# Performance work log

Measured on AMD Instinct MI355X. Metric: run time of the kernel, lower is better.

Reference implementation:

```python
import jax, jax.numpy as jnp
import numpy as np

B, T, E = 4, 2_000_000, 8
C, K, STRIDE = 128, 512, 512
CHUNK, OVERLAP = 64000, 511  # overlap defaults to kernel_size - 1


def _candidate_positions(T):
    """Exact set of window start positions visited by the chunked streaming max.

    Replays the chunk loop of _lowmem_max_over_time: chunk starts advance by
    step = chunk_size - overlap (not a multiple of stride!), and within each
    chunk conv windows start at chunk_start + stride*k.
    """
    step = max(1, CHUNK - OVERLAP)
    pos = []
    start = 0
    while start < T:
        end = min(start + CHUNK, T)
        end_ext = min(end + OVERLAP, T)
        L = end_ext - start
        if L >= K:
            n = (L - K) // STRIDE + 1
            pos.append(start + STRIDE * np.arange(n, dtype=np.int64))
        if end == T:
            break
        start += step
    p = np.unique(np.concatenate(pos))
    return np.clip(p, 0, max(0, T - K))


POS = _candidate_positions(T)                       # [P] static window starts
WIN_IDX = POS[:, None] + np.arange(K, dtype=np.int64)  # [P, K] gather indices


def setup_inputs() -> dict:
    key = jax.random.key(0)
    ks = jax.random.split(key, 5)
    scale = 1.0 / float(np.sqrt(E * K))  # torch Conv1d default init range
    return {
        "x": jax.random.normal(ks[0], (B, T, E), dtype=jnp.float32),
        "w1": jax.random.uniform(ks[1], (C, E, K), jnp.float32, -scale, scale),
        "b1": jax.random.uniform(ks[2], (C,), jnp.float32, -scale, scale),
        "w2": jax.random.uniform(ks[3], (C, E, K), jnp.float32, -scale, scale),
        "b2": jax.random.uniform(ks[4], (C,), jnp.float32, -scale, scale),
    }


def reference(x, w1, b1, w2, b2):
    # Gather every candidate window the chunked scan would see: [B, P, K, E]
    wins = x[:, WIN_IDX, :]
    # Original clones windows under no_grad (stop_grad_input=True): input gets no grad.
    wins = jax.lax.stop_gradient(wins)
    # Gated conv (GLU): conv1(z) * sigmoid(conv2(z)) at each window -> [B, C, P]
    c1 = jnp.einsum('bpke,cek->bcp', wins, w1) + b1[:, None]
    c2 = jnp.einsum('bpke,cek->bcp', wins, w2) + b2[:, None]
    g = c1 * jax.nn.sigmoid(c2)
    # Global max-over-time per (batch, channel); identical value to the
    # running-max pass followed by exact re-evaluation at argmax positions.
    return g.max(axis=-1)  # [B, C]
```

## Files before the change

### kernel.cpp

```cpp
#include <hip/hip_runtime.h>


#define T_LEN 2000000
#define P_CNT 3937
#define M_TOT 15748
#define KD    4096

typedef __attribute__((ext_vector_type(8))) short short8;
typedef __attribute__((ext_vector_type(4))) float f32x4;

static __device__ __forceinline__ unsigned short f2bf(float f) {
    unsigned u = __builtin_bit_cast(unsigned, f);
    unsigned r = (u + 0x7FFFu + ((u >> 16) & 1u)) >> 16;
    return (unsigned short)r;
}

static __device__ __forceinline__ unsigned ordenc(float f) {
    unsigned u = __builtin_bit_cast(unsigned, f);
    return (u & 0x80000000u) ? ~u : (u | 0x80000000u);
}

static __device__ __forceinline__ size_t row_base_bp(int bb, int p) {
    int j, kp;
    if (p < 3875) { j = p / 125; kp = p - j * 125; }
    else          { j = 31;      kp = p - 3875; }
    long pos = (long)j * 63489 + (long)kp * 512;
    return ((size_t)bb * T_LEN + (size_t)pos) * 8u;
}

static __device__ __forceinline__ uint2 cvt4(float4 v) {
    unsigned lo, hi;
    asm("v_cvt_pk_bf16_f32 %0, %1, %2" : "=v"(lo) : "v"(v.x), "v"(v.y));
    asm("v_cvt_pk_bf16_f32 %0, %1, %2" : "=v"(hi) : "v"(v.z), "v"(v.w));
    uint2 u; u.x = lo; u.y = hi;
    return u;
}

__global__ __launch_bounds__(256) void pack_w(const float* __restrict__ w1,
                                              const float* __restrict__ w2,
                                              uint4* __restrict__ Bpf,
                                              unsigned* __restrict__ outu) {
    int c = blockIdx.x * 256 + threadIdx.x;
    if (c < 512) outu[c] = 0u;
    if (c >= 131072) return;
    int l  = c & 63;
    int w  = (c >> 6) & 15;
    int kq = (c >> 10) & 1;
    int ks = c >> 11;
    int cl = l & 15;
    int n  = (cl < 8) ? (w * 8 + cl) : (128 + w * 8 + (cl - 8));
    int kb = ks * 64 + kq * 32 + ((l >> 4) << 3);
    const float* src = (n < 128) ? w1 : w2;
    int cc = n & 127;
    unsigned short h[8];
#pragma unroll
    for (int j = 0; j < 8; ++j) {
        int k = kb + j;
        h[j] = f2bf(src[cc * 4096 + (k & 7) * 512 + (k >> 3)]);
    }
    uint4 v;
    v.x = (unsigned)h[0] | ((unsigned)h[1] << 16);
    v.y = (unsigned)h[2] | ((unsigned)h[3] << 16);
    v.z = (unsigned)h[4] | ((unsigned)h[5] << 16);
    v.w = (unsigned)h[6] | ((unsigned)h[7] << 16);
    Bpf[c] = v;
}

#define LOAD_B(BB, KS)                                                         \
    do {                                                                       \
        _Pragma("unroll")                                                      \
        for (int kq = 0; kq < 2; ++kq)                                         \
            BB[kq] = Bq[((KS) * 2 + kq) * 1024 + bbase];                       \
    } while (0)

#define STEP(KS, BCUR, BNXT)                                                   \
    do {                                                                       \
        const int ks_ = (KS);                                                  \
        const int ksn = (ks_ + 1 < 64) ? ks_ + 1 : 63;                         \
        LOAD_B(BNXT, ksn);                                                     \
        const int ksl = (ks_ + 4 < 64) ? ks_ + 4 : 63;                         \
        float4 aF = *(const float4*)(x + aoff + (size_t)(ksl * 64));           \
        const char* As = smem + (ks_ & 3) * 8192;                              \
        _Pragma("unroll")                                                      \
        for (int kq = 0; kq < 2; ++kq) {                                       \
            short8 b = __builtin_bit_cast(short8, BCUR[kq]);                   \
            _Pragma("unroll")                                                  \
            for (int mf = 0; mf < 4; ++mf) {                                   \
                short8 af = *(const short8*)(As + aro[kq][mf]);                \
                acc[mf] = __builtin_amdgcn_mfma_f32_16x16x32_bf16(             \
                    af, b, acc[mf], 0, 0, 0);                                  \
            }                                                                  \
        }                                                                      \
        *(uint2*)(smem + ((ks_ + 2) & 3) * 8192 + awb) = cvt4(aA);             \
        aA = aB; aB = aF;                                                      \
        asm volatile("s_waitcnt lgkmcnt(0)" ::: "memory");                     \
        __builtin_amdgcn_s_barrier();                                          \
        asm volatile("" ::: "memory");                                         \
    } while (0)

__global__ __launch_bounds__(1024, 4) void gemm_max(const float* __restrict__ x,
                                                    const uint4* __restrict__ Bq,
                                                    const float* __restrict__ b1,
                                                    const float* __restrict__ b2,
                                                    unsigned* __restrict__ outu) {
    __shared__ __align__(16) char smem[32768];

    const int t    = threadIdx.x;
    const int lane = t & 63;
    const int w    = t >> 6;
    const int bid  = blockIdx.x;
    const int bb   = bid / 62;
    const int p0   = (bid % 62) * 64;

    const int rowS = t >> 4;
    const int kcS  = t & 15;
    int pS = p0 + rowS; if (pS > P_CNT - 1) pS = P_CNT - 1;
    const size_t aoff = row_base_bp(bb, pS) + (size_t)(kcS * 4);
    const int    awb  = (rowS * 128 + kcS * 8) ^ ((rowS & 7) << 4);

    int aro[2][2 * 2];
#pragma unroll
    for (int kq = 0; kq < 2; ++kq)
#pragma unroll
        for (int mf = 0; mf < 4; ++mf) {
            int row = mf * 16 + (lane & 15);
            aro[kq][mf] = (row * 128 + kq * 64 + (lane >> 4) * 16)
                          ^ ((row & 7) << 4);
        }

    const int bbase = w * 64 + lane;

#pragma unroll
    for (int pt = 0; pt < 2; ++pt) {
        float4 v = *(const float4*)(x + aoff + pt * 64);
        *(uint2*)(smem + pt * 8192 + awb) = cvt4(v);
    }
    __syncthreads();

    float4 aA = *(const float4*)(x + aoff + 128);
    float4 aB = *(const float4*)(x + aoff + 192);
    uint4 BX[2], BY[2];
    LOAD_B(BX, 0);

    f32x4 acc[4];
#pragma unroll
    for (int mf = 0; mf < 4; ++mf) acc[mf] = (f32x4){0.f, 0.f, 0.f, 0.f};

    for (int ks = 0; ks < 64; ks += 2) {
        STEP(ks, BX, BY);
        STEP(ks + 1, BY, BX);
    }

    const int   cidx = w * 8 + (lane & 7);
    const float bb1  = b1[cidx];
    const float bb2  = b2[cidx];
    float best = -3.4e38f;
#pragma unroll
    for (int mf = 0; mf < 4; ++mf)
#pragma unroll
        for (int q = 0; q < 4; ++q) {
            float v  = acc[mf][q];
            float ov = __shfl_xor(v, 8);
            float c1 = v + bb1;
            float c2 = ov + bb2;
            float g  = c1 / (1.f + __expf(-c2));
            best = fmaxf(best, g);
        }
    best = fmaxf(best, __shfl_xor(best, 16));
    best = fmaxf(best, __shfl_xor(best, 32));
    if (lane < 8)
        atomicMax(&outu[bb * 128 + w * 8 + lane], ordenc(best));
}

__global__ __launch_bounds__(256) void unmap_out(unsigned* __restrict__ outu) {
    int i = blockIdx.x * 256 + threadIdx.x;
    if (i < 512) {
        unsigned u = outu[i];
        outu[i] = (u & 0x80000000u) ? (u ^ 0x80000000u) : ~u;
    }
}

extern "C" void kernel_launch(void* const* d_in, const int* in_sizes, int n_in,
                              void* d_out, int out_size, void* d_ws, size_t ws_size,
                              hipStream_t stream) {
    const float* x  = (const float*)d_in[0];
    const float* w1 = (const float*)d_in[1];
    const float* b1 = (const float*)d_in[2];
    const float* w2 = (const float*)d_in[3];
    const float* b2 = (const float*)d_in[4];

    uint4*    Bpf  = (uint4*)d_ws;
    unsigned* outu = (unsigned*)d_out;

    pack_w<<<dim3(512), dim3(256), 0, stream>>>(w1, w2, Bpf, outu);

    const int nblk = 62 * 4;
    gemm_max<<<dim3(nblk), dim3(1024), 0, stream>>>(x, (const uint4*)Bpf, b1, b2, outu);

    unmap_out<<<dim3(2), dim3(256), 0, stream>>>(outu);
}
```

Baseline: 70.91 us.

## Switch GEMM to 32x32x16 bf16 MFMA with 2x8 wave tiling

Replaces the per-wave four 16x16x32 MFMAs over 64 rows by 8 columns with a single 32x32x16 MFMA accumulator tile covering 32 rows by 32 columns (16 conv1 plus 16 conv2 channels). The weight packing layout, B fragment loads, A LDS offsets and the GLU/max epilogue are rewritten to match. The larger MFMA shape is meant to reduce LDS A-fragment reads per FLOP and instruction issue overhead. In exchange each wave now loads twice as many B fragments per k-step, since B is shared across the two row groups instead of A being shared across waves.

Result: slower. 93.44 us (+31.8%).

```diff
diff --git a/kernel.cpp b/kernel.cpp
--- a/kernel.cpp
+++ b/kernel.cpp
@@ -7,7 +7,7 @@
 #define KD    4096
 
 typedef __attribute__((ext_vector_type(8))) short short8;
-typedef __attribute__((ext_vector_type(4))) float f32x4;
+typedef __attribute__((ext_vector_type(16))) float f32x16;
 
 static __device__ __forceinline__ unsigned short f2bf(float f) {
     unsigned u = __builtin_bit_cast(unsigned, f);
@@ -43,13 +43,14 @@
     int c = blockIdx.x * 256 + threadIdx.x;
     if (c < 512) outu[c] = 0u;
     if (c >= 131072) return;
-    int l  = c & 63;
-    int w  = (c >> 6) & 15;
-    int kq = (c >> 10) & 1;
-    int ks = c >> 11;
-    int cl = l & 15;
-    int n  = (cl < 8) ? (w * 8 + cl) : (128 + w * 8 + (cl - 8));
-    int kb = ks * 64 + kq * 32 + ((l >> 4) << 3);
+    int l    = c & 63;
+    int g    = (c >> 6) & 7;
+    int s    = (c >> 9) & 3;
+    int ks   = c >> 11;
+    int cl   = l & 31;
+    int half = l >> 5;
+    int n  = (cl < 16) ? (g * 16 + cl) : (128 + g * 16 + (cl - 16));
+    int kb = ks * 64 + s * 16 + half * 8;
     const float* src = (n < 128) ? w1 : w2;
     int cc = n & 127;
     unsigned short h[8];
@@ -69,8 +70,8 @@
 #define LOAD_B(BB, KS)                                                         \
     do {                                                                       \
         _Pragma("unroll")                                                      \
-        for (int kq = 0; kq < 2; ++kq)                                         \
-            BB[kq] = Bq[((KS) * 2 + kq) * 1024 + bbase];                       \
+        for (int s = 0; s < 4; ++s)                                            \
+            BB[s] = Bq[((KS) * 4 + s) * 512 + bbase];                          \
     } while (0)
 
 #define STEP(KS, BCUR, BNXT)                                                   \
@@ -82,14 +83,10 @@
         float4 aF = *(const float4*)(x + aoff + (size_t)(ksl * 64));           \
         const char* As = smem + (ks_ & 3) * 8192;                              \
         _Pragma("unroll")                                                      \
-        for (int kq = 0; kq < 2; ++kq) {                                       \
-            short8 b = __builtin_bit_cast(short8, BCUR[kq]);                   \
-            _Pragma("unroll")                                                  \
-            for (int mf = 0; mf < 4; ++mf) {                                   \
-                short8 af = *(const short8*)(As + aro[kq][mf]);                \
-                acc[mf] = __builtin_amdgcn_mfma_f32_16x16x32_bf16(             \
-                    af, b, acc[mf], 0, 0, 0);                                  \
-            }                                                                  \
+        for (int s = 0; s < 4; ++s) {                                          \
+            short8 af = *(const short8*)(As + aro[s]);                         \
+            short8 b  = __builtin_bit_cast(short8, BCUR[s]);                   \
+            acc = __builtin_amdgcn_mfma_f32_32x32x16_bf16(af, b, acc, 0, 0, 0);\
         }                                                                      \
         *(uint2*)(smem + ((ks_ + 2) & 3) * 8192 + awb) = cvt4(aA);             \
         aA = aB; aB = aF;                                                      \
@@ -108,6 +105,8 @@
     const int t    = threadIdx.x;
     const int lane = t & 63;
     const int w    = t >> 6;
+    const int g    = w & 7;
+    const int mg   = w >> 3;
     const int bid  = blockIdx.x;
     const int bb   = bid / 62;
     const int p0   = (bid % 62) * 64;
@@ -118,17 +117,15 @@
     const size_t aoff = row_base_bp(bb, pS) + (size_t)(kcS * 4);
     const int    awb  = (rowS * 128 + kcS * 8) ^ ((rowS & 7) << 4);
 
-    int aro[2][2 * 2];
+    int aro[4];
+    {
+        int row = mg * 32 + (lane & 31);
 #pragma unroll
-    for (int kq = 0; kq < 2; ++kq)
-#pragma unroll
-        for (int mf = 0; mf < 4; ++mf) {
-            int row = mf * 16 + (lane & 15);
-            aro[kq][mf] = (row * 128 + kq * 64 + (lane >> 4) * 16)
-                          ^ ((row & 7) << 4);
-        }
+        for (int s = 0; s < 4; ++s)
+            aro[s] = (row * 128 + s * 32 + (lane >> 5) * 16) ^ ((row & 7) << 4);
+    }
 
-    const int bbase = w * 64 + lane;
+    const int bbase = g * 64 + lane;
 
 #pragma unroll
     for (int pt = 0; pt < 2; ++pt) {
@@ -139,37 +136,35 @@
 
     float4 aA = *(const float4*)(x + aoff + 128);
     float4 aB = *(const float4*)(x + aoff + 192);
-    uint4 BX[2], BY[2];
+    uint4 BX[4], BY[4];
     LOAD_B(BX, 0);
 
-    f32x4 acc[4];
+    f32x16 acc;
 #pragma unroll
-    for (int mf = 0; mf < 4; ++mf) acc[mf] = (f32x4){0.f, 0.f, 0.f, 0.f};
+    for (int i = 0; i < 16; ++i) acc[i] = 0.f;
 
     for (int ks = 0; ks < 64; ks += 2) {
         STEP(ks, BX, BY);
         STEP(ks + 1, BY, BX);
     }
 
-    const int   cidx = w * 8 + (lane & 7);
+    const int   cl   = lane & 31;
+    const int   cidx = g * 16 + (cl & 15);
     const float bb1  = b1[cidx];
     const float bb2  = b2[cidx];
     float best = -3.4e38f;
 #pragma unroll
-    for (int mf = 0; mf < 4; ++mf)
-#pragma unroll
-        for (int q = 0; q < 4; ++q) {
-            float v  = acc[mf][q];
-            float ov = __shfl_xor(v, 8);
-            float c1 = v + bb1;
-            float c2 = ov + bb2;
-            float g  = c1 / (1.f + __expf(-c2));
-            best = fmaxf(best, g);
-        }
-    best = fmaxf(best, __shfl_xor(best, 16));
+    for (int r = 0; r < 16; ++r) {
+        float v  = acc[r];
+        float ov = __shfl_xor(v, 16);
+        float a1 = (cl < 16) ? v : ov;
+        float a2 = (cl < 16) ? ov : v;
+        float gte = (a1 + bb1) / (1.f + __expf(-(a2 + bb2)));
+        best = fmaxf(best, gte);
+    }
     best = fmaxf(best, __shfl_xor(best, 32));
-    if (lane < 8)
-        atomicMax(&outu[bb * 128 + w * 8 + lane], ordenc(best));
+    if (lane < 16)
+        atomicMax(&outu[bb * 128 + g * 16 + lane], ordenc(best));
 }
 
 __global__ __launch_bounds__(256) void unmap_out(unsigned* __restrict__ outu) {
```

## Retile GEMM warps to 2x2 MFMA fragments pairing conv1/conv2 columns

Applied to the files above, without the earlier changes.

Changes the per-wave tiling from 4 M-fragments by one mixed N-fragment (8 conv1 + 8 conv2 channels) to 2 M-fragments by 2 N-fragments (16 conv1 channels and the matching 16 conv2 channels). The weight packing layout is changed to match. Each wave now loads half the A fragments from LDS and two B fragments per k-step, which cuts LDS read traffic. The GLU epilogue no longer needs a cross-lane shuffle to pair c1 with c2. In exchange, B register and global traffic per wave doubles.

Result: slower. 75.54 us (+6.5%).

```diff
diff --git a/kernel.cpp b/kernel.cpp
--- a/kernel.cpp
+++ b/kernel.cpp
@@ -44,11 +44,11 @@
     if (c < 512) outu[c] = 0u;
     if (c >= 131072) return;
     int l  = c & 63;
-    int w  = (c >> 6) & 15;
+    int g  = (c >> 6) & 7;
+    int nf = (c >> 9) & 1;
     int kq = (c >> 10) & 1;
     int ks = c >> 11;
-    int cl = l & 15;
-    int n  = (cl < 8) ? (w * 8 + cl) : (128 + w * 8 + (cl - 8));
+    int n  = nf ? (128 + g * 16 + (l & 15)) : (g * 16 + (l & 15));
     int kb = ks * 64 + kq * 32 + ((l >> 4) << 3);
     const float* src = (n < 128) ? w1 : w2;
     int cc = n & 127;
@@ -70,7 +70,9 @@
     do {                                                                       \
         _Pragma("unroll")                                                      \
         for (int kq = 0; kq < 2; ++kq)                                         \
-            BB[kq] = Bq[((KS) * 2 + kq) * 1024 + bbase];                       \
+            _Pragma("unroll")                                                  \
+            for (int nf = 0; nf < 2; ++nf)                                     \
+                BB[kq][nf] = Bq[((KS) * 4 + kq * 2 + nf) * 512 + bbase];       \
     } while (0)
 
 #define STEP(KS, BCUR, BNXT)                                                   \
@@ -83,13 +85,18 @@
         const char* As = smem + (ks_ & 3) * 8192;                              \
         _Pragma("unroll")                                                      \
         for (int kq = 0; kq < 2; ++kq) {                                       \
-            short8 b = __builtin_bit_cast(short8, BCUR[kq]);                   \
-            _Pragma("unroll")                                                  \
-            for (int mf = 0; mf < 4; ++mf) {                                   \
-                short8 af = *(const short8*)(As + aro[kq][mf]);                \
-                acc[mf] = __builtin_amdgcn_mfma_f32_16x16x32_bf16(             \
-                    af, b, acc[mf], 0, 0, 0);                                  \
-            }                                                                  \
+            short8 af0 = *(const short8*)(As + aro[kq][0]);                    \
+            short8 af1 = *(const short8*)(As + aro[kq][1]);                    \
+            short8 b0  = __builtin_bit_cast(short8, BCUR[kq][0]);              \
+            short8 b1  = __builtin_bit_cast(short8, BCUR[kq][1]);              \
+            acc[0][0] = __builtin_amdgcn_mfma_f32_16x16x32_bf16(               \
+                af0, b0, acc[0][0], 0, 0, 0);                                  \
+            acc[1][0] = __builtin_amdgcn_mfma_f32_16x16x32_bf16(               \
+                af1, b0, acc[1][0], 0, 0, 0);                                  \
+            acc[0][1] = __builtin_amdgcn_mfma_f32_16x16x32_bf16(               \
+                af0, b1, acc[0][1], 0, 0, 0);                                  \
+            acc[1][1] = __builtin_amdgcn_mfma_f32_16x16x32_bf16(               \
+                af1, b1, acc[1][1], 0, 0, 0);                                  \
         }                                                                      \
         *(uint2*)(smem + ((ks_ + 2) & 3) * 8192 + awb) = cvt4(aA);             \
         aA = aB; aB = aF;                                                      \
@@ -108,6 +115,8 @@
     const int t    = threadIdx.x;
     const int lane = t & 63;
     const int w    = t >> 6;
+    const int g    = w & 7;
+    const int mg   = w >> 3;
     const int bid  = blockIdx.x;
     const int bb   = bid / 62;
     const int p0   = (bid % 62) * 64;
@@ -118,17 +127,17 @@
     const size_t aoff = row_base_bp(bb, pS) + (size_t)(kcS * 4);
     const int    awb  = (rowS * 128 + kcS * 8) ^ ((rowS & 7) << 4);
 
-    int aro[2][2 * 2];
+    int aro[2][2];
 #pragma unroll
     for (int kq = 0; kq < 2; ++kq)
 #pragma unroll
-        for (int mf = 0; mf < 4; ++mf) {
-            int row = mf * 16 + (lane & 15);
+        for (int mf = 0; mf < 2; ++mf) {
+            int row = mg * 32 + mf * 16 + (lane & 15);
             aro[kq][mf] = (row * 128 + kq * 64 + (lane >> 4) * 16)
                           ^ ((row & 7) << 4);
         }
 
-    const int bbase = w * 64 + lane;
+    const int bbase = g * 64 + lane;
 
 #pragma unroll
     for (int pt = 0; pt < 2; ++pt) {
@@ -139,37 +148,37 @@
 
     float4 aA = *(const float4*)(x + aoff + 128);
     float4 aB = *(const float4*)(x + aoff + 192);
-    uint4 BX[2], BY[2];
+    uint4 BX[2][2], BY[2][2];
     LOAD_B(BX, 0);
 
-    f32x4 acc[4];
-#pragma unroll
-    for (int mf = 0; mf < 4; ++mf) acc[mf] = (f32x4){0.f, 0.f, 0.f, 0.f};
+    f32x4 acc[2][2];
+#pragma unroll
+    for (int mf = 0; mf < 2; ++mf)
+#pragma unroll
+        for (int nf = 0; nf < 2; ++nf) acc[mf][nf] = (f32x4){0.f, 0.f, 0.f, 0.f};
 
     for (int ks = 0; ks < 64; ks += 2) {
         STEP(ks, BX, BY);
         STEP(ks + 1, BY, BX);
     }
 
-    const int   cidx = w * 8 + (lane & 7);
+    const int   cidx = g * 16 + (lane & 15);
     const float bb1  = b1[cidx];
     const float bb2  = b2[cidx];
     float best = -3.4e38f;
 #pragma unroll
-    for (int mf = 0; mf < 4; ++mf)
+    for (int mf = 0; mf < 2; ++mf)
 #pragma unroll
         for (int q = 0; q < 4; ++q) {
-            float v  = acc[mf][q];
-            float ov = __shfl_xor(v, 8);
-            float c1 = v + bb1;
-            float c2 = ov + bb2;
-            float g  = c1 / (1.f + __expf(-c2));
-            best = fmaxf(best, g);
+            float c1 = acc[mf][0][q] + bb1;
+            float c2 = acc[mf][1][q] + bb2;
+            float gv = c1 / (1.f + __expf(-c2));
+            best = fmaxf(best, gv);
         }
     best = fmaxf(best, __shfl_xor(best, 16));
     best = fmaxf(best, __shfl_xor(best, 32));
-    if (lane < 8)
-        atomicMax(&outu[bb * 128 + w * 8 + lane], ordenc(best));
+    if (lane < 16)
+        atomicMax(&outu[bb * 128 + cidx], ordenc(best));
 }
 
 __global__ __launch_bounds__(256) void unmap_out(unsigned* __restrict__ outu) {
```
